# Kernel optimization log

Measured on AMD Instinct MI355X. Metric: run time of the kernel, lower is better.

Reference implementation:

```python
import jax, jax.numpy as jnp
import numpy as np

N = 20000
E = 640000
R = 8          # num_rels == num_bases (basis regularizer with num_bases=-1)
B = 8
IN_SIZE = 128
HID = 256      # 4 * fea_dimen
FEA = 64
TIME = 2880
POI = 12


def setup_inputs() -> dict:
    key = jax.random.key(0)
    ks = jax.random.split(key, 20)
    s = 0.02
    inp = {
        'src': jax.random.randint(ks[0], (E,), 0, N),
        'dst': jax.random.randint(ks[1], (E,), 0, N),
        'etype': jax.random.randint(ks[2], (E,), 0, R),
        'poi_distribution': jax.random.normal(ks[3], (N, POI), jnp.float32),
        'time_distribution': jax.random.normal(ks[4], (N, TIME), jnp.float32),
        'road_feature': jax.random.normal(ks[5], (N, IN_SIZE), jnp.float32),
        # input projections
        'poi_w': jax.random.normal(ks[6], (POI, FEA), jnp.float32) * s,
        'poi_b': jnp.zeros((FEA,), jnp.float32),
        'time_w': jax.random.normal(ks[7], (TIME, 2 * FEA), jnp.float32) * s,
        'time_b': jnp.zeros((2 * FEA,), jnp.float32),
        'road_w': jax.random.normal(ks[8], (IN_SIZE, FEA), jnp.float32) * s,
        'road_b': jnp.zeros((FEA,), jnp.float32),
        # RelGraphConv layer 1 (basis decomposition)
        'basis1': jax.random.normal(ks[9], (B, HID, HID), jnp.float32) * s,
        'coef1': jax.random.normal(ks[10], (R, B), jnp.float32) * s,
        'loop_w1': jax.random.normal(ks[11], (HID, HID), jnp.float32) * s,
        'bias1': jnp.zeros((HID,), jnp.float32),
        # RelGraphConv layer 2
        'basis2': jax.random.normal(ks[12], (B, HID, HID), jnp.float32) * s,
        'coef2': jax.random.normal(ks[13], (R, B), jnp.float32) * s,
        'loop_w2': jax.random.normal(ks[14], (HID, HID), jnp.float32) * s,
        'bias2': jnp.zeros((HID,), jnp.float32),
    }
    return inp


def _rel_graph_conv(h, src, dst, etype, basis, coef, loop_w, bias):
    # W_r = sum_b coef[r,b] * basis[b]  -> (R, HID, HID), small
    W = jnp.einsum('rb,bio->rio', coef, basis)
    # transform every node by every relation weight, then gather per edge
    y = jnp.einsum('ni,rio->nro', h, W)          # (N, R, HID)
    msgs = y[src, etype]                          # (E, HID) gather
    agg = jax.ops.segment_sum(msgs, dst, num_segments=h.shape[0])  # scatter-sum
    return agg + h @ loop_w + bias


def reference(src, dst, etype, poi_distribution, time_distribution, road_feature,
              poi_w, poi_b, time_w, time_b, road_w, road_b,
              basis1, coef1, loop_w1, bias1, basis2, coef2, loop_w2, bias2):
    poi_feat = poi_distribution @ poi_w + poi_b       # (N, 64)
    time_feat = time_distribution @ time_w + time_b   # (N, 128)
    road_feat = road_feature @ road_w + road_b        # (N, 64)
    feat = jnp.concatenate([poi_feat, time_feat, road_feat], axis=1)  # (N, 256)
    h = _rel_graph_conv(feat, src, dst, etype, basis1, coef1, loop_w1, bias1)
    h = jax.nn.relu(h)  # dropout=0.0 -> identity
    h = _rel_graph_conv(h, src, dst, etype, basis2, coef2, loop_w2, bias2)
    return h
```

## Files before the change

### kernel.cpp

```cpp
#include <hip/hip_runtime.h>

#define NN 20000
#define NE 640000
#define NR 8
#define NB 8
#define HID 256
#define KPOI 12
#define KTIME 2880
#define KROAD 128
#define NK (NN * NR)
#define SPLITK 5
#define KCH (KTIME / SPLITK)

typedef __attribute__((ext_vector_type(8))) short bf8_t;
typedef __attribute__((ext_vector_type(4))) float f4_t;

__device__ inline unsigned short f2bf(float f) {
  unsigned int u = __float_as_uint(f);
  u += 0x7FFF + ((u >> 16) & 1);
  return (unsigned short)(u >> 16);
}
__device__ inline float bf2f(unsigned short h) {
  return __uint_as_float((unsigned int)h << 16);
}

__global__ __launch_bounds__(256) void prep_k(
    const float* __restrict__ loop_w1, const float* __restrict__ loop_w2,
    const float* __restrict__ time_w,
    const float* __restrict__ coef1, const float* __restrict__ basis1,
    const float* __restrict__ coef2, const float* __restrict__ basis2,
    unsigned short* __restrict__ LWT1, unsigned short* __restrict__ LWT2,
    unsigned short* __restrict__ TWT, unsigned short* __restrict__ WT12)
{
  __shared__ unsigned short T[64][66];
  const int b = blockIdx.x;
  if (b < 512) {
    int idx = b * 256 + threadIdx.x;
    int sel = idx >> 16;
    int j = idx & 65535;
    int r = j >> 8, c = j & 255;
    const float* in = sel ? loop_w2 : loop_w1;
    unsigned short* o = sel ? LWT2 : LWT1;
    o[c * HID + r] = f2bf(in[j]);
  } else if (b < 1952) {
    int idx = (b - 512) * 256 + threadIdx.x;
    int r = idx >> 7, c = idx & 127;
    TWT[(size_t)c * KTIME + r] = f2bf(time_w[idx]);
  } else {
    const int bid = b - 1952;
    const int lr = bid >> 4;
    const int it = (bid >> 2) & 3, ot = bid & 3;
    const int i0 = it * 64, o0 = ot * 64;
    const float* coef  = (lr < NR) ? coef1 : coef2;
    const float* basis = (lr < NR) ? basis1 : basis2;
    const int r = lr & 7;
    float cf[NB];
#pragma unroll
    for (int q = 0; q < NB; ++q) cf[q] = coef[r * NB + q];
    const int to = threadIdx.x & 63;
    const int tq = threadIdx.x >> 6;
#pragma unroll
    for (int k = 0; k < 16; ++k) {
      int i_loc = tq * 16 + k;
      int i = i0 + i_loc;
      float acc = 0.f;
#pragma unroll
      for (int q = 0; q < NB; ++q)
        acc += cf[q] * basis[((size_t)(q * HID + i)) * HID + o0 + to];
      T[i_loc][to] = f2bf(acc);
    }
    __syncthreads();
#pragma unroll
    for (int k = 0; k < 16; ++k) {
      int o_loc = tq * 16 + k;
      WT12[(size_t)lr * HID * HID + (size_t)(o0 + o_loc) * HID + i0 + to] =
          T[to][o_loc];
    }
  }
}

#define BK 16
__device__ inline void sgemm_body(
    int M, int Nn, int K,
    const float* __restrict__ A, int lda,
    const float* __restrict__ B, int ldb,
    const float* __restrict__ bias,
    unsigned short* __restrict__ C, int ldc, int brow)
{
  constexpr int BM = 64, BN = 64, TM = 4, TN = 4;
  constexpr int SA = BM + 4;
  constexpr int SB = BN + 4;
  __shared__ float As[BK * SA];
  __shared__ float Bs[BK * SB];
  const int tid = threadIdx.x;
  constexpr int TCOLS = BN / TN;
  const int row0 = (tid / TCOLS) * TM;
  const int col0 = (tid % TCOLS) * TN;

  float acc[TM][TN] = {};

  for (int kb = 0; kb < K; kb += BK) {
    {
      int i = tid;
      int r = i >> 2, q = (i & 3) * 4;
      int grow = brow + r, gk = kb + q;
      if (grow < M && gk + 3 < K) {
        float4 v = *(const float4*)(A + (size_t)grow * lda + gk);
        As[(q + 0) * SA + r] = v.x;
        As[(q + 1) * SA + r] = v.y;
        As[(q + 2) * SA + r] = v.z;
        As[(q + 3) * SA + r] = v.w;
      } else {
#pragma unroll
        for (int j = 0; j < 4; ++j)
          As[(q + j) * SA + r] =
              (grow < M && gk + j < K) ? A[(size_t)grow * lda + gk + j] : 0.f;
      }
    }
    {
      int i = tid;
      int k = i / (BN / 4), cq = (i % (BN / 4)) * 4;
      int gk = kb + k;
      float4 v = {0.f, 0.f, 0.f, 0.f};
      if (gk < K) {
        if (cq + 3 < Nn) {
          v = *(const float4*)(B + (size_t)gk * ldb + cq);
        } else {
#pragma unroll
          for (int j = 0; j < 4; ++j)
            if (cq + j < Nn) (&v.x)[j] = B[(size_t)gk * ldb + cq + j];
        }
      }
      *(float4*)(&Bs[k * SB + cq]) = v;
    }
    __syncthreads();
#pragma unroll
    for (int kk = 0; kk < BK; ++kk) {
      float a[TM], bb[TN];
      *(float4*)(&a[0]) = *(const float4*)(&As[kk * SA + row0]);
      *(float4*)(&bb[0]) = *(const float4*)(&Bs[kk * SB + col0]);
#pragma unroll
      for (int i = 0; i < TM; ++i)
#pragma unroll
        for (int j = 0; j < TN; ++j)
          acc[i][j] += a[i] * bb[j];
    }
    __syncthreads();
  }

  float bcache[TN];
#pragma unroll
  for (int j = 0; j < TN; ++j) bcache[j] = bias[col0 + j];
#pragma unroll
  for (int i = 0; i < TM; ++i) {
    int row = brow + row0 + i;
    if (row >= M) continue;
#pragma unroll
    for (int j = 0; j < TN; ++j)
      C[(size_t)row * ldc + col0 + j] = f2bf(acc[i][j] + bcache[j]);
  }
}

__global__ __launch_bounds__(256) void proj2_k(
    const float* __restrict__ poi_dist, const float* __restrict__ poi_w,
    const float* __restrict__ poi_b,
    const float* __restrict__ road_feat, const float* __restrict__ road_w,
    const float* __restrict__ road_b,
    unsigned short* __restrict__ hbuf)
{
  const int brow = blockIdx.x * 64;
  if (blockIdx.y == 0)
    sgemm_body(NN, 64, KPOI, poi_dist, KPOI, poi_w, 64, poi_b,
               hbuf + 0, HID, brow);
  else
    sgemm_body(NN, 64, KROAD, road_feat, KROAD, road_w, 64, road_b,
               hbuf + 192, HID, brow);
}

__global__ __launch_bounds__(256) void mfma_time_sk(
    const float* __restrict__ A,
    const unsigned short* __restrict__ BT,
    float* __restrict__ TP)
{
  __shared__ __align__(16) char ldsA[32 * 128];
  __shared__ __align__(16) char ldsB[128 * 128];
  const int tid = threadIdx.x;
  const int lane = tid & 63;
  const int w = tid >> 6;
  const int brow = blockIdx.x * 32;
  const int kb0 = blockIdx.y * KCH;

  f4_t acc[2][2];
#pragma unroll
  for (int i = 0; i < 2; ++i)
#pragma unroll
    for (int j = 0; j < 2; ++j) acc[i][j] = (f4_t){0.f, 0.f, 0.f, 0.f};

  for (int kb = kb0; kb < kb0 + KCH; kb += 64) {
    {
      int r = tid >> 3, c8 = tid & 7;
      const float* ap = A + (size_t)(brow + r) * KTIME + kb + c8 * 8;
      f4_t v0 = *(const f4_t*)ap;
      f4_t v1 = *(const f4_t*)(ap + 4);
      unsigned short hh[8];
#pragma unroll
      for (int j = 0; j < 4; ++j) { hh[j] = f2bf(v0[j]); hh[4 + j] = f2bf(v1[j]); }
      *(bf8_t*)(ldsA + r * 128 + ((c8 * 16) ^ ((r & 7) << 4))) = *(bf8_t*)hh;
    }
#pragma unroll
    for (int it = 0; it < 4; ++it) {
      int slot = tid + it * 256;
      int r = slot >> 3, c8 = slot & 7;
      bf8_t v = *(const bf8_t*)(BT + (size_t)r * KTIME + kb + c8 * 8);
      *(bf8_t*)(ldsB + r * 128 + ((c8 * 16) ^ ((r & 7) << 4))) = v;
    }
    __syncthreads();
#pragma unroll
    for (int ks = 0; ks < 2; ++ks) {
      const int kbyte = ks * 64 + (lane >> 4) * 16;
      bf8_t af[2], bfr[2];
#pragma unroll
      for (int mi = 0; mi < 2; ++mi) {
        int m = mi * 16 + (lane & 15);
        af[mi] = *(const bf8_t*)(ldsA + m * 128 + (kbyte ^ ((m & 7) << 4)));
      }
#pragma unroll
      for (int ni = 0; ni < 2; ++ni) {
        int n = w * 32 + ni * 16 + (lane & 15);
        bfr[ni] = *(const bf8_t*)(ldsB + n * 128 + (kbyte ^ ((n & 7) << 4)));
      }
#pragma unroll
      for (int mi = 0; mi < 2; ++mi)
#pragma unroll
        for (int ni = 0; ni < 2; ++ni)
          acc[mi][ni] = __builtin_amdgcn_mfma_f32_16x16x32_bf16(
              af[mi], bfr[ni], acc[mi][ni], 0, 0, 0);
    }
    __syncthreads();
  }

  float* tp = TP + (size_t)blockIdx.y * NN * 128;
  const int rq = (lane >> 4) * 4;
  const int cl = lane & 15;
#pragma unroll
  for (int ni = 0; ni < 2; ++ni) {
    int c = w * 32 + ni * 16 + cl;
#pragma unroll
    for (int mi = 0; mi < 2; ++mi) {
#pragma unroll
      for (int j = 0; j < 4; ++j) {
        int row = brow + mi * 16 + rq + j;
        tp[(size_t)row * 128 + c] = acc[mi][ni][j];
      }
    }
  }
}

__global__ __launch_bounds__(256) void time_finish(
    const float* __restrict__ TP, const float* __restrict__ bias,
    unsigned short* __restrict__ featb) {
  int i = blockIdx.x * 256 + threadIdx.x;
  if (i >= NN * 32) return;
  int row = i >> 5, c4 = (i & 31) * 4;
  f4_t s = *(const f4_t*)(TP + (size_t)row * 128 + c4);
#pragma unroll
  for (int k = 1; k < SPLITK; ++k) {
    f4_t v = *(const f4_t*)(TP + (size_t)k * NN * 128 + (size_t)row * 128 + c4);
    s.x += v.x; s.y += v.y; s.z += v.z; s.w += v.w;
  }
  f4_t b = *(const f4_t*)(bias + c4);
  unsigned short h[4] = {f2bf(s.x + b.x), f2bf(s.y + b.y),
                         f2bf(s.z + b.z), f2bf(s.w + b.w)};
  *(ushort4*)(featb + (size_t)row * 256 + 64 + c4) = *(ushort4*)h;
}

__global__ __launch_bounds__(256) void agg_k(
    const int* __restrict__ offs, const unsigned short* __restrict__ ssrc,
    const unsigned short* __restrict__ hin, unsigned short* __restrict__ Z) {
  int w = (blockIdx.x * 256 + threadIdx.x) >> 6;
  int lane = threadIdx.x & 63;
  if (w >= NR * NN) return;
  int q = w / NN;
  int d = w - q * NN;
  int lo = offs[d * NR + q];
  int hi = offs[d * NR + q + 1];
  f4_t az = {0.f, 0.f, 0.f, 0.f};
  int e = lo;
  for (; e + 4 <= hi; e += 4) {
    int s0 = ssrc[e], s1 = ssrc[e + 1], s2 = ssrc[e + 2], s3 = ssrc[e + 3];
    ushort4 u0 = *(const ushort4*)(hin + (size_t)s0 * HID + lane * 4);
    ushort4 u1 = *(const ushort4*)(hin + (size_t)s1 * HID + lane * 4);
    ushort4 u2 = *(const ushort4*)(hin + (size_t)s2 * HID + lane * 4);
    ushort4 u3 = *(const ushort4*)(hin + (size_t)s3 * HID + lane * 4);
    az.x += (bf2f(u0.x) + bf2f(u1.x)) + (bf2f(u2.x) + bf2f(u3.x));
    az.y += (bf2f(u0.y) + bf2f(u1.y)) + (bf2f(u2.y) + bf2f(u3.y));
    az.z += (bf2f(u0.z) + bf2f(u1.z)) + (bf2f(u2.z) + bf2f(u3.z));
    az.w += (bf2f(u0.w) + bf2f(u1.w)) + (bf2f(u2.w) + bf2f(u3.w));
  }
  for (; e < hi; ++e) {
    int s = ssrc[e];
    ushort4 u = *(const ushort4*)(hin + (size_t)s * HID + lane * 4);
    az.x += bf2f(u.x); az.y += bf2f(u.y);
    az.z += bf2f(u.z); az.w += bf2f(u.w);
  }
  unsigned short hz[4] = {f2bf(az.x), f2bf(az.y), f2bf(az.z), f2bf(az.w)};
  *(ushort4*)(Z + (size_t)w * HID + lane * 4) = *(ushort4*)hz;
}

__global__ __launch_bounds__(512) void gemm_part(
    const unsigned short* __restrict__ hbufA,
    const unsigned short* __restrict__ Z,
    const unsigned short* __restrict__ WT,
    const unsigned short* __restrict__ LWT,
    float* __restrict__ P)
{
  __shared__ __align__(16) char At[32 * 512];
  __shared__ __align__(16) char Bt[256 * 128];
  const int tid = threadIdx.x;
  const int lane = tid & 63;
  const int w = tid >> 6;
  const int wr = w >> 2;
  const int wc = w & 3;
  const int brow = blockIdx.x * 32;
  const int half = blockIdx.y;
  const int sbeg = half ? 5 : 0;
  const int send = half ? 9 : 5;

  f4_t acc[4];
#pragma unroll
  for (int i = 0; i < 4; ++i) acc[i] = (f4_t){0.f, 0.f, 0.f, 0.f};

#pragma unroll 1
  for (int s = sbeg; s < send; ++s) {
    const unsigned short* Asrc = (s == 0) ? hbufA : Z + (size_t)(s - 1) * NN * HID;
    const unsigned short* Wsrc = (s == 0) ? LWT : WT + (size_t)(s - 1) * HID * HID;
#pragma unroll
    for (int it = 0; it < 2; ++it) {
      int slot = tid + it * 512;
      int r = slot >> 5, c16 = slot & 31;
      bf8_t v = *(const bf8_t*)(Asrc + (size_t)(brow + r) * HID + c16 * 8);
      *(bf8_t*)(At + r * 512 + ((c16 * 16) ^ ((r & 7) << 4))) = v;
    }
    __syncthreads();
#pragma unroll 1
    for (int kc = 0; kc < 4; ++kc) {
#pragma unroll
      for (int it = 0; it < 4; ++it) {
        int slot = tid + it * 512;
        int n = slot >> 3, c8 = slot & 7;
        bf8_t v = *(const bf8_t*)(Wsrc + (size_t)n * HID + kc * 64 + c8 * 8);
        *(bf8_t*)(Bt + n * 128 + ((c8 * 16) ^ ((n & 7) << 4))) = v;
      }
      __syncthreads();
#pragma unroll
      for (int ks = 0; ks < 2; ++ks) {
        const int kbyte = ks * 64 + (lane >> 4) * 16;
        int m = wr * 16 + (lane & 15);
        bf8_t af = *(const bf8_t*)(
            At + m * 512 + ((kc * 128 + kbyte) ^ ((m & 7) << 4)));
#pragma unroll
        for (int ni = 0; ni < 4; ++ni) {
          int n = wc * 64 + ni * 16 + (lane & 15);
          bf8_t bfr = *(const bf8_t*)(Bt + n * 128 + (kbyte ^ ((n & 7) << 4)));
          acc[ni] = __builtin_amdgcn_mfma_f32_16x16x32_bf16(af, bfr, acc[ni], 0, 0, 0);
        }
      }
      __syncthreads();
    }
  }

  float* Pout = P + (size_t)half * NN * HID;
  const int rq = (lane >> 4) * 4;
  const int cl = lane & 15;
#pragma unroll
  for (int ni = 0; ni < 4; ++ni) {
    int c = wc * 64 + ni * 16 + cl;
#pragma unroll
    for (int j = 0; j < 4; ++j) {
      int row = brow + wr * 16 + rq + j;
      Pout[(size_t)row * HID + c] = acc[ni][j];
    }
  }
}

template<int RELU>
__global__ __launch_bounds__(256) void combine_k(
    const float* __restrict__ P, const float* __restrict__ bias,
    unsigned short* __restrict__ hb, float* __restrict__ C) {
  int i = blockIdx.x * 256 + threadIdx.x;
  if (i >= NN * 64) return;
  int row = i >> 6, c4 = (i & 63) * 4;
  size_t o = (size_t)row * HID + c4;
  f4_t a = *(const f4_t*)(P + o);
  f4_t b = *(const f4_t*)(P + (size_t)NN * HID + o);
  f4_t bb = *(const f4_t*)(bias + c4);
  f4_t v = {a.x + b.x + bb.x, a.y + b.y + bb.y,
            a.z + b.z + bb.z, a.w + b.w + bb.w};
  if (RELU) {
    unsigned short h[4] = {f2bf(fmaxf(v.x, 0.f)), f2bf(fmaxf(v.y, 0.f)),
                           f2bf(fmaxf(v.z, 0.f)), f2bf(fmaxf(v.w, 0.f))};
    *(ushort4*)(hb + o) = *(ushort4*)h;
  } else {
    *(f4_t*)(C + o) = v;
  }
}

__global__ __launch_bounds__(256) void hist_k(const int* __restrict__ dst,
                                              const int* __restrict__ et,
                                              int* __restrict__ counts) {
  int e = blockIdx.x * 256 + threadIdx.x;
  if (e < NE) atomicAdd(&counts[dst[e] * NR + et[e]], 1);
}

__global__ __launch_bounds__(256) void scan_block(const int* __restrict__ counts,
                                                  int* __restrict__ offs,
                                                  int* __restrict__ bsums) {
  __shared__ int sh[256];
  int base = blockIdx.x * 1024;
  int t = threadIdx.x;
  int v[4];
  int s = 0;
#pragma unroll
  for (int j = 0; j < 4; ++j) {
    int idx = base + t * 4 + j;
    v[j] = (idx < NK) ? counts[idx] : 0;
    s += v[j];
  }
  sh[t] = s;
  __syncthreads();
  for (int off = 1; off < 256; off <<= 1) {
    int x = (t >= off) ? sh[t - off] : 0;
    __syncthreads();
    sh[t] += x;
    __syncthreads();
  }
  int run = sh[t] - s;
#pragma unroll
  for (int j = 0; j < 4; ++j) {
    int idx = base + t * 4 + j;
    if (idx < NK) offs[idx] = run;
    run += v[j];
  }
  if (t == 255) bsums[blockIdx.x] = sh[255];
}

__global__ __launch_bounds__(256) void scan_bsums(int* __restrict__ bsums, int nblk) {
  __shared__ int sh[256];
  int t = threadIdx.x;
  int own = (t < nblk) ? bsums[t] : 0;
  sh[t] = own;
  __syncthreads();
  for (int off = 1; off < 256; off <<= 1) {
    int x = (t >= off) ? sh[t - off] : 0;
    __syncthreads();
    sh[t] += x;
    __syncthreads();
  }
  int ex = sh[t] - own;
  if (t < nblk) bsums[t] = ex;
}

__global__ __launch_bounds__(256) void add_base(int* __restrict__ offs,
                                                const int* __restrict__ bsums,
                                                int* __restrict__ cursor) {
  int idx = blockIdx.x * 256 + threadIdx.x;
  if (idx < NK) {
    int v = offs[idx] + bsums[idx >> 10];
    offs[idx] = v;
    cursor[idx] = v;
  }
  if (idx == NK) offs[NK] = NE;
}

__global__ __launch_bounds__(256) void fill_k(const int* __restrict__ src,
                                              const int* __restrict__ dst,
                                              const int* __restrict__ et,
                                              int* __restrict__ cursor,
                                              unsigned short* __restrict__ ssrc) {
  int e = blockIdx.x * 256 + threadIdx.x;
  if (e < NE) {
    int key = dst[e] * NR + et[e];
    int p = atomicAdd(&cursor[key], 1);
    ssrc[p] = (unsigned short)src[e];
  }
}

extern "C" void kernel_launch(void* const* d_in, const int* in_sizes, int n_in,
                              void* d_out, int out_size, void* d_ws, size_t ws_size,
                              hipStream_t stream) {
  const int*   srcp      = (const int*)d_in[0];
  const int*   dstp      = (const int*)d_in[1];
  const int*   etypep    = (const int*)d_in[2];
  const float* poi_dist  = (const float*)d_in[3];
  const float* time_dist = (const float*)d_in[4];
  const float* road_feat = (const float*)d_in[5];
  const float* poi_w     = (const float*)d_in[6];
  const float* poi_b     = (const float*)d_in[7];
  const float* time_w    = (const float*)d_in[8];
  const float* time_b    = (const float*)d_in[9];
  const float* road_w    = (const float*)d_in[10];
  const float* road_b    = (const float*)d_in[11];
  const float* basis1    = (const float*)d_in[12];
  const float* coef1     = (const float*)d_in[13];
  const float* loop_w1   = (const float*)d_in[14];
  const float* bias1     = (const float*)d_in[15];
  const float* basis2    = (const float*)d_in[16];
  const float* coef2     = (const float*)d_in[17];
  const float* loop_w2   = (const float*)d_in[18];
  const float* bias2     = (const float*)d_in[19];

  float* out = (float*)d_out;

  char* ws = (char*)d_ws;
  unsigned short* WT12   = (unsigned short*)(ws);
  unsigned short* LWT1   = (unsigned short*)(ws + 2097152);
  unsigned short* LWT2   = (unsigned short*)(ws + 2228224);
  unsigned short* TWT    = (unsigned short*)(ws + 2359296);
  unsigned short* hbuf   = (unsigned short*)(ws + 3096576);
  unsigned short* Z      = (unsigned short*)(ws + 13336576);
  float*          TP     = (float*)(ws + 95256576);
  int*            offs   = (int*)  (ws + 146456576);
  int*            bsums  = (int*)  (ws + 147096592);
  unsigned short* ssrc   = (unsigned short*)(ws + 147097616);
  int*            counts = (int*)Z;
  int*            cursor = (int*)TP;
  float*          P      = TP;

  unsigned short* WT1 = WT12;
  unsigned short* WT2 = WT12 + (size_t)NR * HID * HID;

  dim3 blk(256);

  hipMemsetAsync(counts, 0, NK * sizeof(int), stream);
  hist_k<<<NE / 256, blk, 0, stream>>>(dstp, etypep, counts);
  scan_block<<<(NK + 1023) / 1024, blk, 0, stream>>>(counts, offs, bsums);
  scan_bsums<<<1, blk, 0, stream>>>(bsums, (NK + 1023) / 1024);
  add_base<<<(NK + 1 + 255) / 256, blk, 0, stream>>>(offs, bsums, cursor);
  fill_k<<<NE / 256, blk, 0, stream>>>(srcp, dstp, etypep, cursor, ssrc);

  prep_k<<<2208, blk, 0, stream>>>(loop_w1, loop_w2, time_w,
                                   coef1, basis1, coef2, basis2,
                                   LWT1, LWT2, TWT, WT12);

  proj2_k<<<dim3((NN + 63) / 64, 2), blk, 0, stream>>>(
      poi_dist, poi_w, poi_b, road_feat, road_w, road_b, hbuf);
  mfma_time_sk<<<dim3(NN / 32, SPLITK), blk, 0, stream>>>(time_dist, TWT, TP);
  time_finish<<<(NN * 32 + 255) / 256, blk, 0, stream>>>(TP, time_b, hbuf);

  agg_k<<<(NR * NN) / 4, blk, 0, stream>>>(offs, ssrc, hbuf, Z);
  gemm_part<<<dim3(NN / 32, 2), 512, 0, stream>>>(hbuf, Z, WT1, LWT1, P);
  combine_k<1><<<(NN * 64 + 255) / 256, blk, 0, stream>>>(P, bias1, hbuf, nullptr);

  agg_k<<<(NR * NN) / 4, blk, 0, stream>>>(offs, ssrc, hbuf, Z);
  gemm_part<<<dim3(NN / 32, 2), 512, 0, stream>>>(hbuf, Z, WT2, LWT2, P);
  combine_k<0><<<(NN * 64 + 255) / 256, blk, 0, stream>>>(P, bias2, nullptr, out);
}
```

Measured before the change: 462.1 us.

## Concatenate relation aggregates into one K-dim GEMM with fused bias/ReLU epilogue

Result: faster. 419.7 us (-9.2%).

```diff
diff --git a/kernel.cpp b/kernel.cpp
--- a/kernel.cpp
+++ b/kernel.cpp
@@ -9,6 +9,8 @@
 #define KTIME 2880
 #define KROAD 128
 #define NK (NN * NR)
+#define NS 9
+#define KCAT (NS * HID)
 #define SPLITK 5
 #define KCH (KTIME / SPLITK)
 
@@ -29,36 +31,25 @@
     const float* __restrict__ time_w,
     const float* __restrict__ coef1, const float* __restrict__ basis1,
     const float* __restrict__ coef2, const float* __restrict__ basis2,
-    unsigned short* __restrict__ LWT1, unsigned short* __restrict__ LWT2,
-    unsigned short* __restrict__ TWT, unsigned short* __restrict__ WT12)
+    unsigned short* __restrict__ Wc1, unsigned short* __restrict__ Wc2,
+    unsigned short* __restrict__ TWT)
 {
   __shared__ unsigned short T[64][66];
   const int b = blockIdx.x;
-  if (b < 512) {
-    int idx = b * 256 + threadIdx.x;
-    int sel = idx >> 16;
-    int j = idx & 65535;
-    int r = j >> 8, c = j & 255;
-    const float* in = sel ? loop_w2 : loop_w1;
-    unsigned short* o = sel ? LWT2 : LWT1;
-    o[c * HID + r] = f2bf(in[j]);
-  } else if (b < 1952) {
-    int idx = (b - 512) * 256 + threadIdx.x;
-    int r = idx >> 7, c = idx & 127;
-    TWT[(size_t)c * KTIME + r] = f2bf(time_w[idx]);
-  } else {
-    const int bid = b - 1952;
-    const int lr = bid >> 4;
-    const int it = (bid >> 2) & 3, ot = bid & 3;
-    const int i0 = it * 64, o0 = ot * 64;
+  const int to = threadIdx.x & 63;
+  const int tq = threadIdx.x >> 6;
+
+  if (b < 256) {
+    const int lr = b >> 4;
+    const int tile = b & 15;
+    const int i0 = ((tile >> 2) & 3) * 64, o0 = (tile & 3) * 64;
     const float* coef  = (lr < NR) ? coef1 : coef2;
     const float* basis = (lr < NR) ? basis1 : basis2;
+    unsigned short* Wc = (lr < NR) ? Wc1 : Wc2;
     const int r = lr & 7;
     float cf[NB];
 #pragma unroll
     for (int q = 0; q < NB; ++q) cf[q] = coef[r * NB + q];
-    const int to = threadIdx.x & 63;
-    const int tq = threadIdx.x >> 6;
 #pragma unroll
     for (int k = 0; k < 16; ++k) {
       int i_loc = tq * 16 + k;
@@ -73,8 +64,39 @@
 #pragma unroll
     for (int k = 0; k < 16; ++k) {
       int o_loc = tq * 16 + k;
-      WT12[(size_t)lr * HID * HID + (size_t)(o0 + o_loc) * HID + i0 + to] =
-          T[to][o_loc];
+      Wc[(size_t)(o0 + o_loc) * KCAT + r * HID + i0 + to] = T[to][o_loc];
+    }
+  } else if (b < 288) {
+    const int j = b - 256;
+    const int layer = j >> 4;
+    const int tile = j & 15;
+    const int i0 = ((tile >> 2) & 3) * 64, o0 = (tile & 3) * 64;
+    const float* lw = layer ? loop_w2 : loop_w1;
+    unsigned short* Wc = layer ? Wc2 : Wc1;
+#pragma unroll
+    for (int k = 0; k < 16; ++k) {
+      int i_loc = tq * 16 + k;
+      T[i_loc][to] = f2bf(lw[(size_t)(i0 + i_loc) * HID + o0 + to]);
+    }
+    __syncthreads();
+#pragma unroll
+    for (int k = 0; k < 16; ++k) {
+      int o_loc = tq * 16 + k;
+      Wc[(size_t)(o0 + o_loc) * KCAT + NR * HID + i0 + to] = T[to][o_loc];
+    }
+  } else {
+    const int j = b - 288;
+    const int r0 = (j >> 1) * 64, c0 = (j & 1) * 64;
+#pragma unroll
+    for (int k = 0; k < 16; ++k) {
+      int r_loc = tq * 16 + k;
+      T[r_loc][to] = f2bf(time_w[(size_t)(r0 + r_loc) * 128 + c0 + to]);
+    }
+    __syncthreads();
+#pragma unroll
+    for (int k = 0; k < 16; ++k) {
+      int c_loc = tq * 16 + k;
+      TWT[(size_t)(c0 + c_loc) * KTIME + r0 + to] = T[to][c_loc];
     }
   }
 }
@@ -276,12 +298,17 @@
 
 __global__ __launch_bounds__(256) void agg_k(
     const int* __restrict__ offs, const unsigned short* __restrict__ ssrc,
-    const unsigned short* __restrict__ hin, unsigned short* __restrict__ Z) {
+    const unsigned short* __restrict__ hin, unsigned short* __restrict__ Zc) {
   int w = (blockIdx.x * 256 + threadIdx.x) >> 6;
   int lane = threadIdx.x & 63;
-  if (w >= NR * NN) return;
+  if (w >= NS * NN) return;
   int q = w / NN;
   int d = w - q * NN;
+  unsigned short* zp = Zc + (size_t)d * KCAT + q * HID + lane * 4;
+  if (q == NR) {
+    *(ushort4*)zp = *(const ushort4*)(hin + (size_t)d * HID + lane * 4);
+    return;
+  }
   int lo = offs[d * NR + q];
   int hi = offs[d * NR + q + 1];
   f4_t az = {0.f, 0.f, 0.f, 0.f};
@@ -304,104 +331,90 @@
     az.z += bf2f(u.z); az.w += bf2f(u.w);
   }
   unsigned short hz[4] = {f2bf(az.x), f2bf(az.y), f2bf(az.z), f2bf(az.w)};
-  *(ushort4*)(Z + (size_t)w * HID + lane * 4) = *(ushort4*)hz;
-}
-
-__global__ __launch_bounds__(512) void gemm_part(
-    const unsigned short* __restrict__ hbufA,
-    const unsigned short* __restrict__ Z,
-    const unsigned short* __restrict__ WT,
-    const unsigned short* __restrict__ LWT,
-    float* __restrict__ P)
+  *(ushort4*)zp = *(ushort4*)hz;
+}
+
+template<int EPI>
+__global__ __launch_bounds__(512) void gemm_cat(
+    const unsigned short* __restrict__ Zc,
+    const unsigned short* __restrict__ Wc,
+    const float* __restrict__ bias,
+    float* __restrict__ C, unsigned short* __restrict__ hb)
 {
-  __shared__ __align__(16) char At[32 * 512];
+  __shared__ __align__(16) char At[64 * 128];
   __shared__ __align__(16) char Bt[256 * 128];
   const int tid = threadIdx.x;
   const int lane = tid & 63;
   const int w = tid >> 6;
-  const int wr = w >> 2;
-  const int wc = w & 3;
-  const int brow = blockIdx.x * 32;
-  const int half = blockIdx.y;
-  const int sbeg = half ? 5 : 0;
-  const int send = half ? 9 : 5;
-
-  f4_t acc[4];
-#pragma unroll
-  for (int i = 0; i < 4; ++i) acc[i] = (f4_t){0.f, 0.f, 0.f, 0.f};
-
-#pragma unroll 1
-  for (int s = sbeg; s < send; ++s) {
-    const unsigned short* Asrc = (s == 0) ? hbufA : Z + (size_t)(s - 1) * NN * HID;
-    const unsigned short* Wsrc = (s == 0) ? LWT : WT + (size_t)(s - 1) * HID * HID;
-#pragma unroll
-    for (int it = 0; it < 2; ++it) {
+  const int wm = w >> 2;
+  const int wn = w & 3;
+  const int brow = blockIdx.x * 64;
+
+  f4_t acc[2][4];
+#pragma unroll
+  for (int i = 0; i < 2; ++i)
+#pragma unroll
+    for (int j = 0; j < 4; ++j) acc[i][j] = (f4_t){0.f, 0.f, 0.f, 0.f};
+
+  for (int kb = 0; kb < KCAT; kb += 64) {
+    {
+      int r = tid >> 3, c8 = tid & 7;
+      int grow = brow + r;
+      bf8_t v = {0, 0, 0, 0, 0, 0, 0, 0};
+      if (grow < NN) v = *(const bf8_t*)(Zc + (size_t)grow * KCAT + kb + c8 * 8);
+      *(bf8_t*)(At + r * 128 + ((c8 * 16) ^ ((r & 7) << 4))) = v;
+    }
+#pragma unroll
+    for (int it = 0; it < 4; ++it) {
       int slot = tid + it * 512;
-      int r = slot >> 5, c16 = slot & 31;
-      bf8_t v = *(const bf8_t*)(Asrc + (size_t)(brow + r) * HID + c16 * 8);
-      *(bf8_t*)(At + r * 512 + ((c16 * 16) ^ ((r & 7) << 4))) = v;
-    }
-    __syncthreads();
-#pragma unroll 1
-    for (int kc = 0; kc < 4; ++kc) {
-#pragma unroll
-      for (int it = 0; it < 4; ++it) {
-        int slot = tid + it * 512;
-        int n = slot >> 3, c8 = slot & 7;
-        bf8_t v = *(const bf8_t*)(Wsrc + (size_t)n * HID + kc * 64 + c8 * 8);
-        *(bf8_t*)(Bt + n * 128 + ((c8 * 16) ^ ((n & 7) << 4))) = v;
-      }
-      __syncthreads();
-#pragma unroll
-      for (int ks = 0; ks < 2; ++ks) {
-        const int kbyte = ks * 64 + (lane >> 4) * 16;
-        int m = wr * 16 + (lane & 15);
-        bf8_t af = *(const bf8_t*)(
-            At + m * 512 + ((kc * 128 + kbyte) ^ ((m & 7) << 4)));
-#pragma unroll
-        for (int ni = 0; ni < 4; ++ni) {
-          int n = wc * 64 + ni * 16 + (lane & 15);
-          bf8_t bfr = *(const bf8_t*)(Bt + n * 128 + (kbyte ^ ((n & 7) << 4)));
-          acc[ni] = __builtin_amdgcn_mfma_f32_16x16x32_bf16(af, bfr, acc[ni], 0, 0, 0);
-        }
-      }
-      __syncthreads();
-    }
-  }
-
-  float* Pout = P + (size_t)half * NN * HID;
+      int n = slot >> 3, c8 = slot & 7;
+      bf8_t v = *(const bf8_t*)(Wc + (size_t)n * KCAT + kb + c8 * 8);
+      *(bf8_t*)(Bt + n * 128 + ((c8 * 16) ^ ((n & 7) << 4))) = v;
+    }
+    __syncthreads();
+#pragma unroll
+    for (int ks = 0; ks < 2; ++ks) {
+      const int kbyte = ks * 64 + (lane >> 4) * 16;
+      bf8_t af[2], bfr[4];
+#pragma unroll
+      for (int mi = 0; mi < 2; ++mi) {
+        int m = wm * 32 + mi * 16 + (lane & 15);
+        af[mi] = *(const bf8_t*)(At + m * 128 + (kbyte ^ ((m & 7) << 4)));
+      }
+#pragma unroll
+      for (int ni = 0; ni < 4; ++ni) {
+        int n = wn * 64 + ni * 16 + (lane & 15);
+        bfr[ni] = *(const bf8_t*)(Bt + n * 128 + (kbyte ^ ((n & 7) << 4)));
+      }
+#pragma unroll
+      for (int mi = 0; mi < 2; ++mi)
+#pragma unroll
+        for (int ni = 0; ni < 4; ++ni)
+          acc[mi][ni] = __builtin_amdgcn_mfma_f32_16x16x32_bf16(
+              af[mi], bfr[ni], acc[mi][ni], 0, 0, 0);
+    }
+    __syncthreads();
+  }
+
   const int rq = (lane >> 4) * 4;
   const int cl = lane & 15;
 #pragma unroll
   for (int ni = 0; ni < 4; ++ni) {
-    int c = wc * 64 + ni * 16 + cl;
-#pragma unroll
-    for (int j = 0; j < 4; ++j) {
-      int row = brow + wr * 16 + rq + j;
-      Pout[(size_t)row * HID + c] = acc[ni][j];
-    }
-  }
-}
-
-template<int RELU>
-__global__ __launch_bounds__(256) void combine_k(
-    const float* __restrict__ P, const float* __restrict__ bias,
-    unsigned short* __restrict__ hb, float* __restrict__ C) {
-  int i = blockIdx.x * 256 + threadIdx.x;
-  if (i >= NN * 64) return;
-  int row = i >> 6, c4 = (i & 63) * 4;
-  size_t o = (size_t)row * HID + c4;
-  f4_t a = *(const f4_t*)(P + o);
-  f4_t b = *(const f4_t*)(P + (size_t)NN * HID + o);
-  f4_t bb = *(const f4_t*)(bias + c4);
-  f4_t v = {a.x + b.x + bb.x, a.y + b.y + bb.y,
-            a.z + b.z + bb.z, a.w + b.w + bb.w};
-  if (RELU) {
-    unsigned short h[4] = {f2bf(fmaxf(v.x, 0.f)), f2bf(fmaxf(v.y, 0.f)),
-                           f2bf(fmaxf(v.z, 0.f)), f2bf(fmaxf(v.w, 0.f))};
-    *(ushort4*)(hb + o) = *(ushort4*)h;
-  } else {
-    *(f4_t*)(C + o) = v;
+    int c = wn * 64 + ni * 16 + cl;
+    float bv = bias[c];
+#pragma unroll
+    for (int mi = 0; mi < 2; ++mi) {
+#pragma unroll
+      for (int j = 0; j < 4; ++j) {
+        int row = brow + wm * 32 + mi * 16 + rq + j;
+        if (row < NN) {
+          size_t o = (size_t)row * HID + c;
+          float v = acc[mi][ni][j] + bv;
+          if (EPI == 0) C[o] = v;
+          else          hb[o] = f2bf(fmaxf(v, 0.f));
+        }
+      }
+    }
   }
 }
 
@@ -512,22 +525,17 @@
   float* out = (float*)d_out;
 
   char* ws = (char*)d_ws;
-  unsigned short* WT12   = (unsigned short*)(ws);
-  unsigned short* LWT1   = (unsigned short*)(ws + 2097152);
-  unsigned short* LWT2   = (unsigned short*)(ws + 2228224);
+  unsigned short* Wc1    = (unsigned short*)(ws);
+  unsigned short* Wc2    = (unsigned short*)(ws + 1179648);
   unsigned short* TWT    = (unsigned short*)(ws + 2359296);
   unsigned short* hbuf   = (unsigned short*)(ws + 3096576);
-  unsigned short* Z      = (unsigned short*)(ws + 13336576);
-  float*          TP     = (float*)(ws + 95256576);
-  int*            offs   = (int*)  (ws + 146456576);
-  int*            bsums  = (int*)  (ws + 147096592);
-  unsigned short* ssrc   = (unsigned short*)(ws + 147097616);
-  int*            counts = (int*)Z;
+  unsigned short* Zcat   = (unsigned short*)(ws + 13336576);
+  float*          TP     = (float*)(ws + 105496576);
+  int*            offs   = (int*)  (ws + 156696576);
+  int*            bsums  = (int*)  (ws + 157336592);
+  unsigned short* ssrc   = (unsigned short*)(ws + 157337616);
+  int*            counts = (int*)Zcat;
   int*            cursor = (int*)TP;
-  float*          P      = TP;
-
-  unsigned short* WT1 = WT12;
-  unsigned short* WT2 = WT12 + (size_t)NR * HID * HID;
 
   dim3 blk(256);
 
@@ -538,20 +546,18 @@
   add_base<<<(NK + 1 + 255) / 256, blk, 0, stream>>>(offs, bsums, cursor);
   fill_k<<<NE / 256, blk, 0, stream>>>(srcp, dstp, etypep, cursor, ssrc);
 
-  prep_k<<<2208, blk, 0, stream>>>(loop_w1, loop_w2, time_w,
-                                   coef1, basis1, coef2, basis2,
-                                   LWT1, LWT2, TWT, WT12);
+  prep_k<<<378, blk, 0, stream>>>(loop_w1, loop_w2, time_w,
+                                  coef1, basis1, coef2, basis2,
+                                  Wc1, Wc2, TWT);
 
   proj2_k<<<dim3((NN + 63) / 64, 2), blk, 0, stream>>>(
       poi_dist, poi_w, poi_b, road_feat, road_w, road_b, hbuf);
   mfma_time_sk<<<dim3(NN / 32, SPLITK), blk, 0, stream>>>(time_dist, TWT, TP);
   time_finish<<<(NN * 32 + 255) / 256, blk, 0, stream>>>(TP, time_b, hbuf);
 
-  agg_k<<<(NR * NN) / 4, blk, 0, stream>>>(offs, ssrc, hbuf, Z);
-  gemm_part<<<dim3(NN / 32, 2), 512, 0, stream>>>(hbuf, Z, WT1, LWT1, P);
-  combine_k<1><<<(NN * 64 + 255) / 256, blk, 0, stream>>>(P, bias1, hbuf, nullptr);
-
-  agg_k<<<(NR * NN) / 4, blk, 0, stream>>>(offs, ssrc, hbuf, Z);
-  gemm_part<<<dim3(NN / 32, 2), 512, 0, stream>>>(hbuf, Z, WT2, LWT2, P);
-  combine_k<0><<<(NN * 64 + 255) / 256, blk, 0, stream>>>(P, bias2, nullptr, out);
-}
+  agg_k<<<(NS * NN + 3) / 4, blk, 0, stream>>>(offs, ssrc, hbuf, Zcat);
+  gemm_cat<1><<<(NN + 63) / 64, 512, 0, stream>>>(Zcat, Wc1, bias1, nullptr, hbuf);
+
+  agg_k<<<(NS * NN + 3) / 4, blk, 0, stream>>>(offs, ssrc, hbuf, Zcat);
+  gemm_cat<0><<<(NN + 63) / 64, 512, 0, stream>>>(Zcat, Wc2, bias2, out, nullptr);
+}
```
